# Kernel optimization log

Measured on AMD Instinct MI355X. Metric: run time of the kernel, lower is better.

The kernel has to match this reference:

```python
import jax, jax.numpy as jnp
import numpy as np

DIM = 2048
N_HEADS = 16
N_KV_HEADS = 4
HEAD_DIM = DIM // N_HEADS  # 128
N_REP = N_HEADS // N_KV_HEADS  # 4
SEQ = 2048
BATCH = 2


def apply_rope(x, cos, sin):
    # x: [b, s, h, d]; cos/sin: [s, d//2]
    xr = x[..., 0::2]
    xi = x[..., 1::2]
    c = cos[None, :, None, :]
    s = sin[None, :, None, :]
    out_r = xr * c - xi * s
    out_i = xr * s + xi * c
    # interleave back: stack on last axis then flatten
    out = jnp.stack([out_r, out_i], axis=-1)
    return out.reshape(x.shape)


def setup_inputs() -> dict:
    key = jax.random.key(0)
    ks = jax.random.split(key, 7)
    x = jax.random.normal(ks[0], (BATCH, SEQ, DIM), dtype=jnp.float32)
    # realistic rotary tables
    inv_freq = 1.0 / (10000.0 ** (np.arange(0, HEAD_DIM, 2, dtype=np.float32) / HEAD_DIM))
    t = np.arange(SEQ, dtype=np.float32)
    freqs = np.outer(t, inv_freq)  # [S, d//2]
    freqs_cos = jnp.asarray(np.cos(freqs))
    freqs_sin = jnp.asarray(np.sin(freqs))
    sc = 0.02
    Wq = jax.random.normal(ks[1], (DIM, N_HEADS * HEAD_DIM), dtype=jnp.float32) * sc
    Wk = jax.random.normal(ks[2], (DIM, N_KV_HEADS * HEAD_DIM), dtype=jnp.float32) * sc
    Wv = jax.random.normal(ks[3], (DIM, N_KV_HEADS * HEAD_DIM), dtype=jnp.float32) * sc
    Wo = jax.random.normal(ks[4], (N_HEADS * HEAD_DIM, DIM), dtype=jnp.float32) * sc
    return {"x": x, "freqs_cos": freqs_cos, "freqs_sin": freqs_sin,
            "Wq": Wq, "Wk": Wk, "Wv": Wv, "Wo": Wo}


def reference(x, freqs_cos, freqs_sin, Wq, Wk, Wv, Wo):
    b, s, _ = x.shape
    xq = (x @ Wq).reshape(b, s, N_HEADS, HEAD_DIM)
    xk = (x @ Wk).reshape(b, s, N_KV_HEADS, HEAD_DIM)
    xv = (x @ Wv).reshape(b, s, N_KV_HEADS, HEAD_DIM)
    xq = apply_rope(xq, freqs_cos, freqs_sin)
    xk = apply_rope(xk, freqs_cos, freqs_sin)
    # GQA attention without materializing repeated KV:
    # group query heads as [b, g, r, s, d] with g=N_KV_HEADS, r=N_REP
    q = xq.reshape(b, s, N_KV_HEADS, N_REP, HEAD_DIM)
    scale = 1.0 / jnp.sqrt(jnp.float32(HEAD_DIM))
    scores = jnp.einsum('bqgrd,bkgd->bgrqk', q, xk) * scale  # [b,g,r,s,s]
    causal = jnp.tril(jnp.ones((s, s), dtype=bool))
    scores = jnp.where(causal[None, None, None], scores, jnp.finfo(scores.dtype).min)
    probs = jax.nn.softmax(scores, axis=-1)
    out = jnp.einsum('bgrqk,bkgd->bqgrd', probs, xv)  # [b,s,g,r,d]
    out = out.reshape(b, s, N_HEADS * HEAD_DIM)
    return out @ Wo
```

## Files before the change

kernel.cpp:

```cpp
#include <hip/hip_runtime.h>
#include <stdint.h>
#include <stddef.h>

constexpr int BATCH = 2;
constexpr int SEQ   = 2048;
constexpr int EMB   = 2048;
constexpr int HEADS = 16;
constexpr int GQA   = 4;
constexpr int HDIM  = 128;
constexpr int NQKV  = 3072;
constexpr int VOFF  = 2560;
constexpr int MROWS = BATCH * SEQ;

typedef _Float16 half8  __attribute__((ext_vector_type(8)));
typedef _Float16 half4v __attribute__((ext_vector_type(4)));
typedef float    floatx4 __attribute__((ext_vector_type(4)));

__device__ __forceinline__ void st_c(float* p, float v)    { *p = v; }
__device__ __forceinline__ void st_c(_Float16* p, float v) { *p = (_Float16)v; }

__global__ void cast_x_kernel(const float* __restrict__ x, _Float16* __restrict__ xh) {
    int i = (blockIdx.x * 256 + threadIdx.x) * 4;
    float4 v = *(const float4*)(x + i);
    half4v h;
    h[0] = (_Float16)v.x; h[1] = (_Float16)v.y; h[2] = (_Float16)v.z; h[3] = (_Float16)v.w;
    *(half4v*)(xh + i) = h;
}

__global__ void transpose_cast(const float* __restrict__ in, _Float16* __restrict__ out,
                               int R, int C) {
    __shared__ float tile[32][33];
    int cb = blockIdx.x * 32, rb = blockIdx.y * 32;
    int tx = threadIdx.x, ty = threadIdx.y;
    #pragma unroll
    for (int j = 0; j < 32; j += 8)
        tile[ty + j][tx] = in[(size_t)(rb + ty + j) * C + (cb + tx)];
    __syncthreads();
    #pragma unroll
    for (int j = 0; j < 32; j += 8)
        out[(size_t)(cb + ty + j) * R + (rb + tx)] = (_Float16)tile[tx][ty + j];
}

template <typename CT>
__global__ __launch_bounds__(256) void gemm_bt(const _Float16* __restrict__ A,
                                               const _Float16* __restrict__ Bt,
                                               CT* __restrict__ C,
                                               int M, int N, int K) {
    constexpr int LDT = 40;
    __shared__ _Float16 As[128 * LDT];
    __shared__ _Float16 Bs[128 * LDT];
    const int tid  = threadIdx.x;
    const int bm   = blockIdx.y * 128, bn = blockIdx.x * 128;
    const int lane = tid & 63, wid = tid >> 6;
    const int wr   = wid >> 1, wc = wid & 1;
    const int qd   = lane >> 4, m15 = lane & 15;

    const int sr = tid >> 2;
    const int sc = (tid & 3) * 8;
    const _Float16* Ag  = A  + (size_t)(bm + sr) * K + sc;
    const _Float16* Ag2 = Ag + (size_t)64 * K;
    const _Float16* Bg  = Bt + (size_t)(bn + sr) * K + sc;
    const _Float16* Bg2 = Bg + (size_t)64 * K;

    half8 a0 = *(const half8*)(Ag);
    half8 a1 = *(const half8*)(Ag2);
    half8 b0 = *(const half8*)(Bg);
    half8 b1 = *(const half8*)(Bg2);

    floatx4 acc[4][4] = {};

    _Float16* AsW  = As + sr * LDT + sc;
    _Float16* AsW2 = AsW + 64 * LDT;
    _Float16* BsW  = Bs + sr * LDT + sc;
    _Float16* BsW2 = BsW + 64 * LDT;
    const _Float16* AsR = As + (wr * 64 + m15) * LDT + qd * 8;
    const _Float16* BsR = Bs + (wc * 64 + m15) * LDT + qd * 8;

    for (int k0 = 0; k0 < K; k0 += 32) {
        *(half8*)AsW  = a0;  *(half8*)AsW2 = a1;
        *(half8*)BsW  = b0;  *(half8*)BsW2 = b1;
        __syncthreads();
        if (k0 + 32 < K) {
            a0 = *(const half8*)(Ag  + k0 + 32);
            a1 = *(const half8*)(Ag2 + k0 + 32);
            b0 = *(const half8*)(Bg  + k0 + 32);
            b1 = *(const half8*)(Bg2 + k0 + 32);
        }
        half8 af[4], bf[4];
        #pragma unroll
        for (int i = 0; i < 4; i++) af[i] = *(const half8*)(AsR + i * 16 * LDT);
        #pragma unroll
        for (int i = 0; i < 4; i++) bf[i] = *(const half8*)(BsR + i * 16 * LDT);
        #pragma unroll
        for (int mi = 0; mi < 4; mi++)
            #pragma unroll
            for (int ni = 0; ni < 4; ni++)
                acc[mi][ni] = __builtin_amdgcn_mfma_f32_16x16x32_f16(af[mi], bf[ni], acc[mi][ni], 0, 0, 0);
        __syncthreads();
    }

    #pragma unroll
    for (int mi = 0; mi < 4; mi++)
        #pragma unroll
        for (int ni = 0; ni < 4; ni++)
            #pragma unroll
            for (int r = 0; r < 4; r++) {
                int row = bm + wr * 64 + mi * 16 + qd * 4 + r;
                int col = bn + wc * 64 + ni * 16 + m15;
                st_c(&C[(size_t)row * N + col], acc[mi][ni][r]);
            }
}

__global__ void rope_inplace(_Float16* __restrict__ qkv, const float* __restrict__ fc,
                             const float* __restrict__ fs) {
    int t   = blockIdx.x * 256 + threadIdx.x;
    int row = t / 1280;
    int p   = t - row * 1280;
    int s   = row & (SEQ - 1);
    int col, i;
    if (p < 1024) { col = 2 * p;                 i = p & 63; }
    else          { col = EMB + 2 * (p - 1024);  i = (p - 1024) & 63; }
    float c  = fc[s * 64 + i];
    float sn = fs[s * 64 + i];
    _Float16* ptr = qkv + (size_t)row * NQKV + col;
    float xr = (float)ptr[0], xi = (float)ptr[1];
    ptr[0] = (_Float16)(xr * c - xi * sn);
    ptr[1] = (_Float16)(xr * sn + xi * c);
}

__global__ void transpose_v(const _Float16* __restrict__ qkv, _Float16* __restrict__ vt) {
    __shared__ _Float16 tile[32][33];
    int sb = blockIdx.x * 32, db = blockIdx.y * 32;
    int bg = blockIdx.z;
    int tx = threadIdx.x, ty = threadIdx.y;
    const _Float16* src = qkv + (size_t)(bg >> 2) * SEQ * NQKV + VOFF + (bg & 3) * HDIM;
    #pragma unroll
    for (int j = 0; j < 32; j += 8)
        tile[ty + j][tx] = src[(size_t)(sb + ty + j) * NQKV + db + tx];
    __syncthreads();
    _Float16* dst = vt + (size_t)bg * HDIM * SEQ;
    #pragma unroll
    for (int j = 0; j < 32; j += 8)
        dst[(size_t)(db + ty + j) * SEQ + sb + tx] = tile[tx][ty + j];
}

__global__ __launch_bounds__(256, 3) void flash_attn(const _Float16* __restrict__ qkv,
                                                     const _Float16* __restrict__ vt,
                                                     _Float16* __restrict__ ob) {
    const int sidx = 127 - blockIdx.x;
    const int g    = blockIdx.y;
    const int b    = blockIdx.z;
    const int tid  = threadIdx.x;
    const int lane = tid & 63, wid = tid >> 6;
    const int h    = g * 4 + wid;
    const int qd   = lane >> 4, m15 = lane & 15;

    __shared__ _Float16 Ks[64 * 136];
    __shared__ _Float16 Vs[144 * 72];
    __shared__ _Float16 Ps[4][16 * 72];

    const int q0     = sidx * 16;
    const int ktLast = sidx >> 2;

    for (int idx = tid; idx < 16 * 72; idx += 256) {
        int rr = idx / 72, cc = idx - rr * 72;
        Vs[(128 + rr) * 72 + cc] = (rr == 0) ? (_Float16)1.0f : (_Float16)0.0f;
    }

    half8 qf[4];
    {
        const _Float16* qb = qkv + (size_t)(b * SEQ + q0 + m15) * NQKV + h * HDIM + qd * 8;
        #pragma unroll
        for (int kc = 0; kc < 4; kc++) qf[kc] = *(const half8*)(qb + kc * 32);
    }

    floatx4 o[9] = {};
    float mr[4];
    #pragma unroll
    for (int r = 0; r < 4; r++) mr[r] = -__builtin_inff();
    const float scale = 0.08838834764831845f;

    const _Float16* kg = qkv + (size_t)(b * SEQ) * NQKV + EMB + g * HDIM;
    const _Float16* vg = vt + (size_t)(b * GQA + g) * HDIM * SEQ;
    _Float16* pw = Ps[wid];

    const int kr0 = tid >> 4, kcc = (tid & 15) * 8;
    const int vr0 = tid >> 3, vcc = (tid & 7) * 8;

    half8 kreg[4], vreg[4];
    #pragma unroll
    for (int it = 0; it < 4; ++it)
        kreg[it] = *(const half8*)(kg + (size_t)(kr0 + it * 16) * NQKV + kcc);
    #pragma unroll
    for (int it = 0; it < 4; ++it)
        vreg[it] = *(const half8*)(vg + (size_t)(vr0 + it * 32) * SEQ + vcc);

    for (int kt = 0; kt <= ktLast; ++kt) {
        const int k0 = kt * 64;
        __syncthreads();
        #pragma unroll
        for (int it = 0; it < 4; ++it)
            *(half8*)(&Ks[(kr0 + it * 16) * 136 + kcc]) = kreg[it];
        #pragma unroll
        for (int it = 0; it < 4; ++it)
            *(half8*)(&Vs[(vr0 + it * 32) * 72 + vcc]) = vreg[it];
        __syncthreads();

        if (kt < ktLast) {
            const int k0n = k0 + 64;
            #pragma unroll
            for (int it = 0; it < 4; ++it)
                kreg[it] = *(const half8*)(kg + (size_t)(k0n + kr0 + it * 16) * NQKV + kcc);
            #pragma unroll
            for (int it = 0; it < 4; ++it)
                vreg[it] = *(const half8*)(vg + (size_t)(vr0 + it * 32) * SEQ + k0n + vcc);
        }

        floatx4 sa[4] = {};
        #pragma unroll
        for (int nt = 0; nt < 4; ++nt)
            #pragma unroll
            for (int kc = 0; kc < 4; ++kc) {
                half8 kf = *(const half8*)(&Ks[(nt * 16 + m15) * 136 + kc * 32 + qd * 8]);
                sa[nt] = __builtin_amdgcn_mfma_f32_16x16x32_f16(qf[kc], kf, sa[nt], 0, 0, 0);
            }

        const bool diag = (kt == ktLast);
        float mn[4], al[4];
        #pragma unroll
        for (int r = 0; r < 4; r++) {
            const int rowg = q0 + qd * 4 + r;
            #pragma unroll
            for (int nt = 0; nt < 4; nt++) {
                float v = sa[nt][r] * scale;
                if (diag && (k0 + nt * 16 + m15 > rowg)) v = -__builtin_inff();
                sa[nt][r] = v;
            }
            float mt = fmaxf(fmaxf(sa[0][r], sa[1][r]), fmaxf(sa[2][r], sa[3][r]));
            mt = fmaxf(mt, __shfl_xor(mt, 1, 64));
            mt = fmaxf(mt, __shfl_xor(mt, 2, 64));
            mt = fmaxf(mt, __shfl_xor(mt, 4, 64));
            mt = fmaxf(mt, __shfl_xor(mt, 8, 64));
            float mnew = fmaxf(mr[r], mt);
            al[r] = __expf(mr[r] - mnew);
            mn[r] = mnew; mr[r] = mnew;
        }

        #pragma unroll
        for (int r = 0; r < 4; r++) {
            #pragma unroll
            for (int nt = 0; nt < 4; nt++) {
                float p = __expf(sa[nt][r] - mn[r]);
                pw[(qd * 4 + r) * 72 + nt * 16 + m15] = (_Float16)p;
            }
            #pragma unroll
            for (int dt = 0; dt < 9; dt++) o[dt][r] *= al[r];
        }

        half8 pf0 = *(const half8*)(&pw[m15 * 72 + qd * 8]);
        half8 pf1 = *(const half8*)(&pw[m15 * 72 + 32 + qd * 8]);
        #pragma unroll
        for (int dt = 0; dt < 9; dt++) {
            half8 vf0 = *(const half8*)(&Vs[(dt * 16 + m15) * 72 + qd * 8]);
            half8 vf1 = *(const half8*)(&Vs[(dt * 16 + m15) * 72 + 32 + qd * 8]);
            o[dt] = __builtin_amdgcn_mfma_f32_16x16x32_f16(pf0, vf0, o[dt], 0, 0, 0);
            o[dt] = __builtin_amdgcn_mfma_f32_16x16x32_f16(pf1, vf1, o[dt], 0, 0, 0);
        }
    }

    float linv[4];
    #pragma unroll
    for (int r = 0; r < 4; r++) {
        float l = __shfl(o[8][r], lane & 48, 64);
        linv[r] = 1.0f / l;
    }
    _Float16* od = ob + (size_t)(b * SEQ + q0) * EMB + h * HDIM;
    #pragma unroll
    for (int dt = 0; dt < 8; dt++)
        #pragma unroll
        for (int r = 0; r < 4; r++)
            od[(size_t)(qd * 4 + r) * EMB + dt * 16 + m15] = (_Float16)(o[dt][r] * linv[r]);
}

extern "C" void kernel_launch(void* const* d_in, const int* in_sizes, int n_in,
                              void* d_out, int out_size, void* d_ws, size_t ws_size,
                              hipStream_t stream) {
    (void)in_sizes; (void)n_in; (void)out_size; (void)ws_size;
    const float* x  = (const float*)d_in[0];
    const float* fc = (const float*)d_in[1];
    const float* fs = (const float*)d_in[2];
    const float* Wq = (const float*)d_in[3];
    const float* Wk = (const float*)d_in[4];
    const float* Wv = (const float*)d_in[5];
    const float* Wo = (const float*)d_in[6];
    float* out = (float*)d_out;

    _Float16* Xb   = (_Float16*)d_ws;
    _Float16* Wqkv = Xb   + (size_t)MROWS * EMB;
    _Float16* WoT  = Wqkv + (size_t)NQKV * EMB;
    _Float16* C1   = WoT  + (size_t)EMB * EMB;
    _Float16* Vt   = Wqkv;
    _Float16* Ob   = Xb;

    dim3 tb(32, 8);
    cast_x_kernel<<<MROWS * EMB / 1024, 256, 0, stream>>>(x, Xb);
    transpose_cast<<<dim3(EMB / 32, EMB / 32), tb, 0, stream>>>(Wq, Wqkv, EMB, EMB);
    transpose_cast<<<dim3(512 / 32, EMB / 32), tb, 0, stream>>>(Wk, Wqkv + (size_t)EMB * EMB, EMB, 512);
    transpose_cast<<<dim3(512 / 32, EMB / 32), tb, 0, stream>>>(Wv, Wqkv + (size_t)VOFF * EMB, EMB, 512);
    transpose_cast<<<dim3(EMB / 32, EMB / 32), tb, 0, stream>>>(Wo, WoT, EMB, EMB);

    gemm_bt<_Float16><<<dim3(NQKV / 128, MROWS / 128), 256, 0, stream>>>(Xb, Wqkv, C1, MROWS, NQKV, EMB);
    rope_inplace<<<MROWS * 1280 / 256, 256, 0, stream>>>(C1, fc, fs);
    transpose_v<<<dim3(SEQ / 32, HDIM / 32, BATCH * GQA), tb, 0, stream>>>(C1, Vt);
    flash_attn<<<dim3(128, GQA, BATCH), 256, 0, stream>>>(C1, Vt, Ob);
    gemm_bt<float><<<dim3(EMB / 128, MROWS / 128), 256, 0, stream>>>(Ob, WoT, out, MROWS, EMB, EMB);
}
```

Before: 373.9 us.

## Use direct global-to-LDS loads with XOR swizzle, fuse RoPE into GEMM, widen attention tiles

The GEMM now loads tiles straight into LDS through global_load_lds with an XOR-swizzled layout instead of padded register staging. The RoPE kernel is folded into the QKV GEMM epilogue using a lane shuffle. Flash attention now processes 32 query rows per wave (two 16-row subtiles) so each K/V tile is reused twice, with swizzled LDS and direct loads. The cost is that register prefetch overlap is gone: each load is followed immediately by a barrier. Occupancy also drops to 2 blocks per SM and the grid is halved.

New measurement: 387.6 us. 3.7% more time.

```diff
diff --git a/kernel.cpp b/kernel.cpp
--- a/kernel.cpp
+++ b/kernel.cpp
@@ -19,6 +19,12 @@
 __device__ __forceinline__ void st_c(float* p, float v)    { *p = v; }
 __device__ __forceinline__ void st_c(_Float16* p, float v) { *p = (_Float16)v; }
 
+__device__ __forceinline__ void gld16(const _Float16* g, _Float16* l) {
+    __builtin_amdgcn_global_load_lds(
+        (const __attribute__((address_space(1))) void*)g,
+        (__attribute__((address_space(3))) void*)l, 16, 0, 0);
+}
+
 __global__ void cast_x_kernel(const float* __restrict__ x, _Float16* __restrict__ xh) {
     int i = (blockIdx.x * 256 + threadIdx.x) * 4;
     float4 v = *(const float4*)(x + i);
@@ -41,62 +47,62 @@
         out[(size_t)(cb + ty + j) * R + (rb + tx)] = (_Float16)tile[tx][ty + j];
 }
 
-template <typename CT>
-__global__ __launch_bounds__(256) void gemm_bt(const _Float16* __restrict__ A,
+template <typename CT, bool ROPE>
+__global__ __launch_bounds__(256) void gemm_as(const _Float16* __restrict__ A,
                                                const _Float16* __restrict__ Bt,
                                                CT* __restrict__ C,
-                                               int M, int N, int K) {
-    constexpr int LDT = 40;
-    __shared__ _Float16 As[128 * LDT];
-    __shared__ _Float16 Bs[128 * LDT];
+                                               int M, int N, int K,
+                                               const float* __restrict__ fc,
+                                               const float* __restrict__ fs) {
+    __shared__ _Float16 As[128 * 32];
+    __shared__ _Float16 Bs[128 * 32];
     const int tid  = threadIdx.x;
     const int bm   = blockIdx.y * 128, bn = blockIdx.x * 128;
     const int lane = tid & 63, wid = tid >> 6;
     const int wr   = wid >> 1, wc = wid & 1;
     const int qd   = lane >> 4, m15 = lane & 15;
 
-    const int sr = tid >> 2;
-    const int sc = (tid & 3) * 8;
-    const _Float16* Ag  = A  + (size_t)(bm + sr) * K + sc;
-    const _Float16* Ag2 = Ag + (size_t)64 * K;
-    const _Float16* Bg  = Bt + (size_t)(bn + sr) * K + sc;
-    const _Float16* Bg2 = Bg + (size_t)64 * K;
-
-    half8 a0 = *(const half8*)(Ag);
-    half8 a1 = *(const half8*)(Ag2);
-    half8 b0 = *(const half8*)(Bg);
-    half8 b1 = *(const half8*)(Bg2);
+    const int l4 = lane >> 2, c4 = lane & 3;
+    const int gcol = (c4 ^ (l4 & 3)) * 8;
+    const _Float16* AgRow[2]; const _Float16* BgRow[2];
+    _Float16* AsB[2]; _Float16* BsB[2];
+    #pragma unroll
+    for (int j = 0; j < 2; j++) {
+        int t = wid * 2 + j;
+        int row = t * 16 + l4;
+        AgRow[j] = A  + (size_t)(bm + row) * K + gcol;
+        BgRow[j] = Bt + (size_t)(bn + row) * K + gcol;
+        AsB[j] = As + t * 512;
+        BsB[j] = Bs + t * 512;
+    }
+    const _Float16* AsR[4]; const _Float16* BsR[4];
+    #pragma unroll
+    for (int i = 0; i < 4; i++) {
+        int ra = wr * 64 + i * 16 + m15;
+        int rb2 = wc * 64 + i * 16 + m15;
+        AsR[i] = As + ra * 32 + ((qd ^ (ra & 3)) * 8);
+        BsR[i] = Bs + rb2 * 32 + ((qd ^ (rb2 & 3)) * 8);
+    }
 
     floatx4 acc[4][4] = {};
 
-    _Float16* AsW  = As + sr * LDT + sc;
-    _Float16* AsW2 = AsW + 64 * LDT;
-    _Float16* BsW  = Bs + sr * LDT + sc;
-    _Float16* BsW2 = BsW + 64 * LDT;
-    const _Float16* AsR = As + (wr * 64 + m15) * LDT + qd * 8;
-    const _Float16* BsR = Bs + (wc * 64 + m15) * LDT + qd * 8;
-
     for (int k0 = 0; k0 < K; k0 += 32) {
-        *(half8*)AsW  = a0;  *(half8*)AsW2 = a1;
-        *(half8*)BsW  = b0;  *(half8*)BsW2 = b1;
         __syncthreads();
-        if (k0 + 32 < K) {
-            a0 = *(const half8*)(Ag  + k0 + 32);
-            a1 = *(const half8*)(Ag2 + k0 + 32);
-            b0 = *(const half8*)(Bg  + k0 + 32);
-            b1 = *(const half8*)(Bg2 + k0 + 32);
-        }
+        gld16(AgRow[0] + k0, AsB[0]);
+        gld16(AgRow[1] + k0, AsB[1]);
+        gld16(BgRow[0] + k0, BsB[0]);
+        gld16(BgRow[1] + k0, BsB[1]);
+        __syncthreads();
         half8 af[4], bf[4];
         #pragma unroll
-        for (int i = 0; i < 4; i++) af[i] = *(const half8*)(AsR + i * 16 * LDT);
-        #pragma unroll
-        for (int i = 0; i < 4; i++) bf[i] = *(const half8*)(BsR + i * 16 * LDT);
+        for (int i = 0; i < 4; i++) af[i] = *(const half8*)(AsR[i]);
+        #pragma unroll
+        for (int i = 0; i < 4; i++) bf[i] = *(const half8*)(BsR[i]);
         #pragma unroll
         for (int mi = 0; mi < 4; mi++)
             #pragma unroll
             for (int ni = 0; ni < 4; ni++)
                 acc[mi][ni] = __builtin_amdgcn_mfma_f32_16x16x32_f16(af[mi], bf[ni], acc[mi][ni], 0, 0, 0);
-        __syncthreads();
     }
 
     #pragma unroll
@@ -107,25 +113,17 @@
             for (int r = 0; r < 4; r++) {
                 int row = bm + wr * 64 + mi * 16 + qd * 4 + r;
                 int col = bn + wc * 64 + ni * 16 + m15;
-                st_c(&C[(size_t)row * N + col], acc[mi][ni][r]);
-            }
-}
-
-__global__ void rope_inplace(_Float16* __restrict__ qkv, const float* __restrict__ fc,
-                             const float* __restrict__ fs) {
-    int t   = blockIdx.x * 256 + threadIdx.x;
-    int row = t / 1280;
-    int p   = t - row * 1280;
-    int s   = row & (SEQ - 1);
-    int col, i;
-    if (p < 1024) { col = 2 * p;                 i = p & 63; }
-    else          { col = EMB + 2 * (p - 1024);  i = (p - 1024) & 63; }
-    float c  = fc[s * 64 + i];
-    float sn = fs[s * 64 + i];
-    _Float16* ptr = qkv + (size_t)row * NQKV + col;
-    float xr = (float)ptr[0], xi = (float)ptr[1];
-    ptr[0] = (_Float16)(xr * c - xi * sn);
-    ptr[1] = (_Float16)(xr * sn + xi * c);
+                float v = acc[mi][ni][r];
+                if (ROPE && col < VOFF) {
+                    int si = row & (SEQ - 1);
+                    int fi = (col >> 1) & 63;
+                    float c  = fc[si * 64 + fi];
+                    float sn = fs[si * 64 + fi];
+                    float other = __shfl_xor(v, 1, 64);
+                    v = (m15 & 1) ? (v * c + other * sn) : (v * c - other * sn);
+                }
+                st_c(&C[(size_t)row * N + col], v);
+            }
 }
 
 __global__ void transpose_v(const _Float16* __restrict__ qkv, _Float16* __restrict__ vt) {
@@ -144,10 +142,10 @@
         dst[(size_t)(db + ty + j) * SEQ + sb + tx] = tile[tx][ty + j];
 }
 
-__global__ __launch_bounds__(256, 3) void flash_attn(const _Float16* __restrict__ qkv,
+__global__ __launch_bounds__(256, 2) void flash_attn(const _Float16* __restrict__ qkv,
                                                      const _Float16* __restrict__ vt,
                                                      _Float16* __restrict__ ob) {
-    const int sidx = 127 - blockIdx.x;
+    const int sidx = 63 - blockIdx.x;
     const int g    = blockIdx.y;
     const int b    = blockIdx.z;
     const int tid  = threadIdx.x;
@@ -155,131 +153,143 @@
     const int h    = g * 4 + wid;
     const int qd   = lane >> 4, m15 = lane & 15;
 
-    __shared__ _Float16 Ks[64 * 136];
-    __shared__ _Float16 Vs[144 * 72];
-    __shared__ _Float16 Ps[4][16 * 72];
-
-    const int q0     = sidx * 16;
-    const int ktLast = sidx >> 2;
-
-    for (int idx = tid; idx < 16 * 72; idx += 256) {
-        int rr = idx / 72, cc = idx - rr * 72;
-        Vs[(128 + rr) * 72 + cc] = (rr == 0) ? (_Float16)1.0f : (_Float16)0.0f;
-    }
-
-    half8 qf[4];
-    {
-        const _Float16* qb = qkv + (size_t)(b * SEQ + q0 + m15) * NQKV + h * HDIM + qd * 8;
-        #pragma unroll
-        for (int kc = 0; kc < 4; kc++) qf[kc] = *(const half8*)(qb + kc * 32);
-    }
-
-    floatx4 o[9] = {};
-    float mr[4];
-    #pragma unroll
-    for (int r = 0; r < 4; r++) mr[r] = -__builtin_inff();
+    __shared__ _Float16 Ks[64 * 128];
+    __shared__ _Float16 Vs[144 * 64];
+    __shared__ _Float16 Ps[4][32 * 64];
+
+    const int q0     = sidx * 32;
+    const int ktLast = sidx >> 1;
+
+    for (int t = tid; t < 16 * 64; t += 256)
+        Vs[128 * 64 + t] = (t < 64) ? (_Float16)1.0f : (_Float16)0.0f;
+
+    half8 qf[2][4];
+    #pragma unroll
+    for (int su = 0; su < 2; su++) {
+        const _Float16* qb = qkv + (size_t)(b * SEQ + q0 + su * 16 + m15) * NQKV + h * HDIM + qd * 8;
+        #pragma unroll
+        for (int kc = 0; kc < 4; kc++) qf[su][kc] = *(const half8*)(qb + kc * 32);
+    }
+
+    floatx4 o[2][9] = {};
+    float mr[2][4];
+    #pragma unroll
+    for (int su = 0; su < 2; su++)
+        #pragma unroll
+        for (int r = 0; r < 4; r++) mr[su][r] = -__builtin_inff();
     const float scale = 0.08838834764831845f;
 
     const _Float16* kg = qkv + (size_t)(b * SEQ) * NQKV + EMB + g * HDIM;
     const _Float16* vg = vt + (size_t)(b * GQA + g) * HDIM * SEQ;
     _Float16* pw = Ps[wid];
 
-    const int kr0 = tid >> 4, kcc = (tid & 15) * 8;
-    const int vr0 = tid >> 3, vcc = (tid & 7) * 8;
-
-    half8 kreg[4], vreg[4];
-    #pragma unroll
-    for (int it = 0; it < 4; ++it)
-        kreg[it] = *(const half8*)(kg + (size_t)(kr0 + it * 16) * NQKV + kcc);
-    #pragma unroll
-    for (int it = 0; it < 4; ++it)
-        vreg[it] = *(const half8*)(vg + (size_t)(vr0 + it * 32) * SEQ + vcc);
+    const int kl = lane >> 4, kc16 = lane & 15;
+    const int vl = lane >> 3, vc8  = lane & 7;
+    const _Float16* kgp[4]; _Float16* ksb[4];
+    const _Float16* vgp[4]; _Float16* vsb[4];
+    #pragma unroll
+    for (int j = 0; j < 4; j++) {
+        int t = wid * 4 + j;
+        int kr = t * 4 + kl;
+        kgp[j] = kg + (size_t)kr * NQKV + ((kc16 ^ (kr & 15)) * 8);
+        ksb[j] = Ks + t * 512;
+        int vr = t * 8 + vl;
+        vgp[j] = vg + (size_t)vr * SEQ + ((vc8 ^ (vr & 7)) * 8);
+        vsb[j] = Vs + t * 512;
+    }
 
     for (int kt = 0; kt <= ktLast; ++kt) {
         const int k0 = kt * 64;
         __syncthreads();
         #pragma unroll
-        for (int it = 0; it < 4; ++it)
-            *(half8*)(&Ks[(kr0 + it * 16) * 136 + kcc]) = kreg[it];
-        #pragma unroll
-        for (int it = 0; it < 4; ++it)
-            *(half8*)(&Vs[(vr0 + it * 32) * 72 + vcc]) = vreg[it];
+        for (int j = 0; j < 4; j++) gld16(kgp[j] + (size_t)k0 * NQKV, ksb[j]);
+        #pragma unroll
+        for (int j = 0; j < 4; j++) gld16(vgp[j] + k0, vsb[j]);
         __syncthreads();
 
-        if (kt < ktLast) {
-            const int k0n = k0 + 64;
-            #pragma unroll
-            for (int it = 0; it < 4; ++it)
-                kreg[it] = *(const half8*)(kg + (size_t)(k0n + kr0 + it * 16) * NQKV + kcc);
-            #pragma unroll
-            for (int it = 0; it < 4; ++it)
-                vreg[it] = *(const half8*)(vg + (size_t)(vr0 + it * 32) * SEQ + k0n + vcc);
+        floatx4 sa[2][4] = {};
+        #pragma unroll
+        for (int nt = 0; nt < 4; ++nt) {
+            const int kr = nt * 16 + m15;
+            #pragma unroll
+            for (int kc = 0; kc < 4; ++kc) {
+                half8 kf = *(const half8*)(&Ks[kr * 128 + (((kc * 4 + qd) ^ (kr & 15)) * 8)]);
+                sa[0][nt] = __builtin_amdgcn_mfma_f32_16x16x32_f16(qf[0][kc], kf, sa[0][nt], 0, 0, 0);
+                sa[1][nt] = __builtin_amdgcn_mfma_f32_16x16x32_f16(qf[1][kc], kf, sa[1][nt], 0, 0, 0);
+            }
         }
 
-        floatx4 sa[4] = {};
-        #pragma unroll
-        for (int nt = 0; nt < 4; ++nt)
-            #pragma unroll
-            for (int kc = 0; kc < 4; ++kc) {
-                half8 kf = *(const half8*)(&Ks[(nt * 16 + m15) * 136 + kc * 32 + qd * 8]);
-                sa[nt] = __builtin_amdgcn_mfma_f32_16x16x32_f16(qf[kc], kf, sa[nt], 0, 0, 0);
-            }
-
         const bool diag = (kt == ktLast);
-        float mn[4], al[4];
+        #pragma unroll
+        for (int su = 0; su < 2; su++) {
+            float mn[4], al[4];
+            #pragma unroll
+            for (int r = 0; r < 4; r++) {
+                const int rowg = q0 + su * 16 + qd * 4 + r;
+                #pragma unroll
+                for (int nt = 0; nt < 4; nt++) {
+                    float v = sa[su][nt][r] * scale;
+                    if (diag && (k0 + nt * 16 + m15 > rowg)) v = -__builtin_inff();
+                    sa[su][nt][r] = v;
+                }
+                float mt = fmaxf(fmaxf(sa[su][0][r], sa[su][1][r]), fmaxf(sa[su][2][r], sa[su][3][r]));
+                mt = fmaxf(mt, __shfl_xor(mt, 1, 64));
+                mt = fmaxf(mt, __shfl_xor(mt, 2, 64));
+                mt = fmaxf(mt, __shfl_xor(mt, 4, 64));
+                mt = fmaxf(mt, __shfl_xor(mt, 8, 64));
+                float mnew = fmaxf(mr[su][r], mt);
+                al[r] = __expf(mr[su][r] - mnew);
+                mn[r] = mnew; mr[su][r] = mnew;
+            }
+            #pragma unroll
+            for (int r = 0; r < 4; r++) {
+                const int prow = su * 16 + qd * 4 + r;
+                #pragma unroll
+                for (int nt = 0; nt < 4; nt++) {
+                    float p = __expf(sa[su][nt][r] - mn[r]);
+                    int chunk = (nt * 2 + (m15 >> 3)) ^ (prow & 7);
+                    pw[prow * 64 + chunk * 8 + (m15 & 7)] = (_Float16)p;
+                }
+                #pragma unroll
+                for (int dt = 0; dt < 9; dt++) o[su][dt][r] *= al[r];
+            }
+        }
+
+        half8 pf[2][2];
+        #pragma unroll
+        for (int su = 0; su < 2; su++)
+            #pragma unroll
+            for (int kc = 0; kc < 2; kc++) {
+                int prow = su * 16 + m15;
+                pf[su][kc] = *(const half8*)(&pw[prow * 64 + (((kc * 4 + qd) ^ (prow & 7)) * 8)]);
+            }
+        #pragma unroll
+        for (int dt = 0; dt < 9; dt++) {
+            #pragma unroll
+            for (int kc = 0; kc < 2; kc++) {
+                int vr = dt * 16 + m15;
+                half8 vf = *(const half8*)(&Vs[vr * 64 + (((kc * 4 + qd) ^ (vr & 7)) * 8)]);
+                o[0][dt] = __builtin_amdgcn_mfma_f32_16x16x32_f16(pf[0][kc], vf, o[0][dt], 0, 0, 0);
+                o[1][dt] = __builtin_amdgcn_mfma_f32_16x16x32_f16(pf[1][kc], vf, o[1][dt], 0, 0, 0);
+            }
+        }
+    }
+
+    #pragma unroll
+    for (int su = 0; su < 2; su++) {
+        float linv[4];
         #pragma unroll
         for (int r = 0; r < 4; r++) {
-            const int rowg = q0 + qd * 4 + r;
-            #pragma unroll
-            for (int nt = 0; nt < 4; nt++) {
-                float v = sa[nt][r] * scale;
-                if (diag && (k0 + nt * 16 + m15 > rowg)) v = -__builtin_inff();
-                sa[nt][r] = v;
-            }
-            float mt = fmaxf(fmaxf(sa[0][r], sa[1][r]), fmaxf(sa[2][r], sa[3][r]));
-            mt = fmaxf(mt, __shfl_xor(mt, 1, 64));
-            mt = fmaxf(mt, __shfl_xor(mt, 2, 64));
-            mt = fmaxf(mt, __shfl_xor(mt, 4, 64));
-            mt = fmaxf(mt, __shfl_xor(mt, 8, 64));
-            float mnew = fmaxf(mr[r], mt);
-            al[r] = __expf(mr[r] - mnew);
-            mn[r] = mnew; mr[r] = mnew;
+            float l = __shfl(o[su][8][r], lane & 48, 64);
+            linv[r] = 1.0f / l;
         }
-
-        #pragma unroll
-        for (int r = 0; r < 4; r++) {
-            #pragma unroll
-            for (int nt = 0; nt < 4; nt++) {
-                float p = __expf(sa[nt][r] - mn[r]);
-                pw[(qd * 4 + r) * 72 + nt * 16 + m15] = (_Float16)p;
-            }
-            #pragma unroll
-            for (int dt = 0; dt < 9; dt++) o[dt][r] *= al[r];
-        }
-
-        half8 pf0 = *(const half8*)(&pw[m15 * 72 + qd * 8]);
-        half8 pf1 = *(const half8*)(&pw[m15 * 72 + 32 + qd * 8]);
-        #pragma unroll
-        for (int dt = 0; dt < 9; dt++) {
-            half8 vf0 = *(const half8*)(&Vs[(dt * 16 + m15) * 72 + qd * 8]);
-            half8 vf1 = *(const half8*)(&Vs[(dt * 16 + m15) * 72 + 32 + qd * 8]);
-            o[dt] = __builtin_amdgcn_mfma_f32_16x16x32_f16(pf0, vf0, o[dt], 0, 0, 0);
-            o[dt] = __builtin_amdgcn_mfma_f32_16x16x32_f16(pf1, vf1, o[dt], 0, 0, 0);
-        }
-    }
-
-    float linv[4];
-    #pragma unroll
-    for (int r = 0; r < 4; r++) {
-        float l = __shfl(o[8][r], lane & 48, 64);
-        linv[r] = 1.0f / l;
-    }
-    _Float16* od = ob + (size_t)(b * SEQ + q0) * EMB + h * HDIM;
-    #pragma unroll
-    for (int dt = 0; dt < 8; dt++)
-        #pragma unroll
-        for (int r = 0; r < 4; r++)
-            od[(size_t)(qd * 4 + r) * EMB + dt * 16 + m15] = (_Float16)(o[dt][r] * linv[r]);
+        _Float16* od = ob + (size_t)(b * SEQ + q0 + su * 16) * EMB + h * HDIM;
+        #pragma unroll
+        for (int dt = 0; dt < 8; dt++)
+            #pragma unroll
+            for (int r = 0; r < 4; r++)
+                od[(size_t)(qd * 4 + r) * EMB + dt * 16 + m15] = (_Float16)(o[su][dt][r] * linv[r]);
+    }
 }
 
 extern "C" void kernel_launch(void* const* d_in, const int* in_sizes, int n_in,
@@ -309,9 +319,10 @@
     transpose_cast<<<dim3(512 / 32, EMB / 32), tb, 0, stream>>>(Wv, Wqkv + (size_t)VOFF * EMB, EMB, 512);
     transpose_cast<<<dim3(EMB / 32, EMB / 32), tb, 0, stream>>>(Wo, WoT, EMB, EMB);
 
-    gemm_bt<_Float16><<<dim3(NQKV / 128, MROWS / 128), 256, 0, stream>>>(Xb, Wqkv, C1, MROWS, NQKV, EMB);
-    rope_inplace<<<MROWS * 1280 / 256, 256, 0, stream>>>(C1, fc, fs);
+    gemm_as<_Float16, true><<<dim3(NQKV / 128, MROWS / 128), 256, 0, stream>>>(
+        Xb, Wqkv, C1, MROWS, NQKV, EMB, fc, fs);
     transpose_v<<<dim3(SEQ / 32, HDIM / 32, BATCH * GQA), tb, 0, stream>>>(C1, Vt);
-    flash_attn<<<dim3(128, GQA, BATCH), 256, 0, stream>>>(C1, Vt, Ob);
-    gemm_bt<float><<<dim3(EMB / 128, MROWS / 128), 256, 0, stream>>>(Ob, WoT, out, MROWS, EMB, EMB);
-}
+    flash_attn<<<dim3(64, GQA, BATCH), 256, 0, stream>>>(C1, Vt, Ob);
+    gemm_as<float, false><<<dim3(EMB / 128, MROWS / 128), 256, 0, stream>>>(
+        Ob, WoT, out, MROWS, EMB, EMB, nullptr, nullptr);
+}
```
